# Kernel tuning notes

Measured on AMD Instinct MI355X. Metric: run time of the kernel, lower is better.

## Reference

```python
import jax, jax.numpy as jnp
import numpy as np

EPS = 1e-5
N_DOMAINS = 16


def setup_inputs() -> dict:
    key = jax.random.key(0)
    k1, k2 = jax.random.split(key)
    N, C = 65536, 512
    X = jax.random.normal(k1, (N, C), dtype=jnp.float32)
    d = jax.random.randint(k2, (N,), 0, N_DOMAINS, dtype=jnp.int32)
    parameter_t = jnp.ones((1,), dtype=jnp.float32)
    fm_mean = jnp.zeros((1, C), dtype=jnp.float32)
    gamma = jnp.ones((N_DOMAINS, C), dtype=jnp.float32)
    beta = jnp.zeros((N_DOMAINS, C), dtype=jnp.float32)
    return {"X": X, "d": d, "parameter_t": parameter_t, "fm_mean": fm_mean,
            "gamma": gamma, "beta": beta}


def reference(X, d, parameter_t, fm_mean, gamma, beta):
    # Per-domain batch normalization with dispatch/combine expressed as
    # segment reductions + gather (mathematically identical to the torch
    # loop over unique domains with mask/concat/scatter-back).
    n_domains = gamma.shape[0]
    ones = jnp.ones((X.shape[0],), dtype=X.dtype)
    cnt = jax.ops.segment_sum(ones, d, num_segments=n_domains)          # [D]
    cnt = jnp.maximum(cnt, 1.0)[:, None]                                 # [D,1]
    s = jax.ops.segment_sum(X, d, num_segments=n_domains)               # [D,C]
    sq = jax.ops.segment_sum(X * X, d, num_segments=n_domains)          # [D,C]
    mean = s / cnt                                                       # [D,C]
    var = sq / cnt - mean * mean                                         # biased var, [D,C]
    inv = jax.lax.rsqrt(var + EPS)                                       # [D,C]
    # gather per-sample domain stats and normalize (scatter-back is implicit)
    y = (X - mean[d]) * inv[d] * gamma[d] + beta[d]
    return y
```

## Files before the change

### kernel.cpp

```cpp
#include <hip/hip_runtime.h>

constexpr int   ND_  = 16;
constexpr int   C_   = 512;
constexpr float EPS_ = 1e-5f;

__global__ __launch_bounds__(256) void k_stats(
    const float2* __restrict__ X2, const int* __restrict__ dd,
    float* __restrict__ part_sum, float* __restrict__ part_sq,
    int* __restrict__ pcnt, int rows_per_chunk, int N) {
  __shared__ float2 ssum[2][ND_][128];
  __shared__ float2 ssq [2][ND_][128];
  __shared__ int    sd[256];
  __shared__ int    scnt[ND_];

  const int tid  = threadIdx.x;
  const int g    = tid >> 7;
  const int lane = tid & 127;
  const int bx   = blockIdx.x;
  const int by   = blockIdx.y;

  for (int i = tid; i < 2 * ND_ * 128; i += 256) {
    ((float2*)ssum)[i] = make_float2(0.f, 0.f);
    ((float2*)ssq )[i] = make_float2(0.f, 0.f);
  }
  if (tid < ND_) scnt[tid] = 0;
  __syncthreads();

  const int r0 = by * rows_per_chunk;
  const int r1 = min(N, r0 + rows_per_chunk);
  const int nr = r1 - r0;

  for (int i = tid; i < nr; i += 256) {
    const int v = dd[r0 + i];
    sd[i] = v;
    if (bx == 0) atomicAdd(&scnt[v], 1);
  }
  __syncthreads();

  const int jr0 = g * 128;
  const int jr1 = min(nr, jr0 + 128);
  const int ch2 = bx * 128 + lane;
  #pragma unroll 8
  for (int j = jr0; j < jr1; ++j) {
    const int    dn = sd[j];
    const float2 v  = X2[(size_t)(r0 + j) * (C_ / 2) + ch2];
    float2 a = ssum[g][dn][lane];
    a.x += v.x; a.y += v.y;
    ssum[g][dn][lane] = a;
    float2 b = ssq[g][dn][lane];
    b.x = fmaf(v.x, v.x, b.x);
    b.y = fmaf(v.y, v.y, b.y);
    ssq[g][dn][lane] = b;
  }
  __syncthreads();

  if (tid < 128) {
    #pragma unroll
    for (int dom = 0; dom < ND_; ++dom) {
      float2 a = ssum[0][dom][tid], a1 = ssum[1][dom][tid];
      a.x += a1.x; a.y += a1.y;
      ssum[0][dom][tid] = a;
      float2 b = ssq[0][dom][tid], b1 = ssq[1][dom][tid];
      b.x += b1.x; b.y += b1.y;
      ssq[0][dom][tid] = b;
    }
  }
  __syncthreads();

  float2* ps = (float2*)part_sum;
  float2* pq = (float2*)part_sq;
  const size_t base = (size_t)by * ND_ * (C_ / 2);
  for (int idx = tid; idx < ND_ * 128; idx += 256) {
    const int dom = idx >> 7;
    const int ln  = idx & 127;
    const size_t o = base + dom * (C_ / 2) + bx * 128 + ln;
    ps[o] = ssum[0][dom][ln];
    pq[o] = ssq [0][dom][ln];
  }
  if (bx == 0 && tid < ND_) pcnt[by * ND_ + tid] = scnt[tid];
}

__global__ __launch_bounds__(256) void k_finalize(
    const float* __restrict__ part_sum, const float* __restrict__ part_sq,
    const int* __restrict__ pcnt, const float* __restrict__ gamma,
    const float* __restrict__ beta, float* __restrict__ scale,
    float* __restrict__ shift, int nchunk) {
  __shared__ float ssum[8][32];
  __shared__ float ssq [8][32];
  __shared__ int   scnt[8];

  const int t     = threadIdx.x;
  const int lane  = t & 31;
  const int seg   = t >> 5;
  const int out0  = blockIdx.x * 32;
  const int gid   = out0 + lane;
  const int dom   = out0 >> 9;
  const int c     = gid & (C_ - 1);
  const int cpl   = (nchunk + 7) / 8;

  float s = 0.f, q = 0.f;
  int   cn = 0;
  for (int k = 0; k < cpl; ++k) {
    const int ch = seg * cpl + k;
    if (ch < nchunk) {
      const size_t o = ((size_t)ch * ND_ + dom) * C_ + c;
      s += part_sum[o];
      q += part_sq[o];
      cn += pcnt[ch * ND_ + dom];
    }
  }
  ssum[seg][lane] = s;
  ssq [seg][lane] = q;
  if (lane == 0) scnt[seg] = cn;
  __syncthreads();

  if (t < 32) {
    float S = 0.f, Q = 0.f;
    #pragma unroll
    for (int sg = 0; sg < 8; ++sg) { S += ssum[sg][t]; Q += ssq[sg][t]; }
    int CN = 0;
    #pragma unroll
    for (int sg = 0; sg < 8; ++sg) CN += scnt[sg];
    const float fc   = fmaxf((float)CN, 1.f);
    const float mean = S / fc;
    const float var  = Q / fc - mean * mean;
    const float inv  = rsqrtf(var + EPS_);
    const int   g    = out0 + t;
    const float sc   = inv * gamma[g];
    scale[g] = sc;
    shift[g] = fmaf(-mean, sc, beta[g]);
  }
}

__global__ __launch_bounds__(256) void k_norm(
    const float4* __restrict__ X4, const int* __restrict__ dd,
    const float4* __restrict__ scale4, const float4* __restrict__ shift4,
    float4* __restrict__ Y4, int total4) {
  int i = blockIdx.x * 256 + threadIdx.x;
  const int stride = gridDim.x * 256;
  for (; i < total4; i += stride) {
    const int n  = i >> 7;
    const int c4 = i & 127;
    const int dn = dd[n];
    const float4 x  = X4[i];
    const float4 sc = scale4[dn * (C_ / 4) + c4];
    const float4 sh = shift4[dn * (C_ / 4) + c4];
    float4 y;
    y.x = fmaf(x.x, sc.x, sh.x);
    y.y = fmaf(x.y, sc.y, sh.y);
    y.z = fmaf(x.z, sc.z, sh.z);
    y.w = fmaf(x.w, sc.w, sh.w);
    Y4[i] = y;
  }
}

extern "C" void kernel_launch(void* const* d_in, const int* in_sizes, int n_in,
                              void* d_out, int out_size, void* d_ws, size_t ws_size,
                              hipStream_t stream) {
  const float* X     = (const float*)d_in[0];
  const int*   dd    = (const int*)  d_in[1];
  const float* gamma = (const float*)d_in[4];
  const float* beta  = (const float*)d_in[5];
  float*       out   = (float*)d_out;

  const int N      = in_sizes[1];
  const int rpc    = 256;
  const int NCHUNK = (N + rpc - 1) / rpc;

  float* part_sum = out;
  float* part_sq  = out + (size_t)NCHUNK * ND_ * C_;
  int*   pcnt     = (int*)(part_sq + (size_t)NCHUNK * ND_ * C_);
  float* scale = (float*)d_ws;
  float* shift = scale + ND_ * C_;

  dim3 g1(2, NCHUNK);
  k_stats<<<g1, 256, 0, stream>>>((const float2*)X, dd, part_sum, part_sq,
                                  pcnt, rpc, N);
  k_finalize<<<(ND_ * C_) / 32, 256, 0, stream>>>(
      part_sum, part_sq, pcnt, gamma, beta, scale, shift, NCHUNK);

  const int total4 = N * (C_ / 4);
  int blocks = (total4 + 255) / 256;
  if (blocks > 2048) blocks = 2048;
  k_norm<<<blocks, 256, 0, stream>>>((const float4*)X, dd,
                                     (const float4*)scale,
                                     (const float4*)shift,
                                     (float4*)out, total4);
}
```

Measured before the change: 84.52 us.

## Replace per-chunk partial buffers with replicated atomic accumulators

Statistics blocks now atomically add their per-domain sums and squared sums into 8 replicated accumulator copies instead of writing full per-chunk partials. The finalize kernel only reduces 8 copies and reads a global count. This removes tens of megabytes of partial-sum writes and reads between kernels. In exchange it adds a memset, contention on atomics, and nondeterministic float summation order.

```diff
diff --git a/kernel.cpp b/kernel.cpp
--- a/kernel.cpp
+++ b/kernel.cpp
@@ -3,11 +3,12 @@
 constexpr int   ND_  = 16;
 constexpr int   C_   = 512;
 constexpr float EPS_ = 1e-5f;
+constexpr int   NREP = 8;
 
 __global__ __launch_bounds__(256) void k_stats(
     const float2* __restrict__ X2, const int* __restrict__ dd,
-    float* __restrict__ part_sum, float* __restrict__ part_sq,
-    int* __restrict__ pcnt, int rows_per_chunk, int N) {
+    float* __restrict__ acc_sum, float* __restrict__ acc_sq,
+    int* __restrict__ cnt, int rows_per_chunk, int N) {
   __shared__ float2 ssum[2][ND_][128];
   __shared__ float2 ssq [2][ND_][128];
   __shared__ int    sd[256];
@@ -67,69 +68,39 @@
   }
   __syncthreads();
 
-  float2* ps = (float2*)part_sum;
-  float2* pq = (float2*)part_sq;
-  const size_t base = (size_t)by * ND_ * (C_ / 2);
-  for (int idx = tid; idx < ND_ * 128; idx += 256) {
-    const int dom = idx >> 7;
-    const int ln  = idx & 127;
-    const size_t o = base + dom * (C_ / 2) + bx * 128 + ln;
-    ps[o] = ssum[0][dom][ln];
-    pq[o] = ssq [0][dom][ln];
+  float* asum = acc_sum + (size_t)(by & (NREP - 1)) * ND_ * C_;
+  float* asq  = acc_sq  + (size_t)(by & (NREP - 1)) * ND_ * C_;
+  for (int idx = tid; idx < ND_ * 256; idx += 256) {
+    const int dom = idx >> 8;
+    const int ci  = idx & 255;
+    const float sv = ((const float*)ssum[0][dom])[ci];
+    const float qv = ((const float*)ssq [0][dom])[ci];
+    unsafeAtomicAdd(&asum[dom * C_ + bx * 256 + ci], sv);
+    unsafeAtomicAdd(&asq [dom * C_ + bx * 256 + ci], qv);
   }
-  if (bx == 0 && tid < ND_) pcnt[by * ND_ + tid] = scnt[tid];
+  if (bx == 0 && tid < ND_) atomicAdd(&cnt[tid], scnt[tid]);
 }
 
-__global__ __launch_bounds__(256) void k_finalize(
-    const float* __restrict__ part_sum, const float* __restrict__ part_sq,
-    const int* __restrict__ pcnt, const float* __restrict__ gamma,
+__global__ __launch_bounds__(128) void k_finalize(
+    const float* __restrict__ acc_sum, const float* __restrict__ acc_sq,
+    const int* __restrict__ cnt, const float* __restrict__ gamma,
     const float* __restrict__ beta, float* __restrict__ scale,
-    float* __restrict__ shift, int nchunk) {
-  __shared__ float ssum[8][32];
-  __shared__ float ssq [8][32];
-  __shared__ int   scnt[8];
-
-  const int t     = threadIdx.x;
-  const int lane  = t & 31;
-  const int seg   = t >> 5;
-  const int out0  = blockIdx.x * 32;
-  const int gid   = out0 + lane;
-  const int dom   = out0 >> 9;
-  const int c     = gid & (C_ - 1);
-  const int cpl   = (nchunk + 7) / 8;
-
+    float* __restrict__ shift) {
+  const int gid = blockIdx.x * 128 + threadIdx.x;
+  const int dom = gid >> 9;
   float s = 0.f, q = 0.f;
-  int   cn = 0;
-  for (int k = 0; k < cpl; ++k) {
-    const int ch = seg * cpl + k;
-    if (ch < nchunk) {
-      const size_t o = ((size_t)ch * ND_ + dom) * C_ + c;
-      s += part_sum[o];
-      q += part_sq[o];
-      cn += pcnt[ch * ND_ + dom];
-    }
+  #pragma unroll
+  for (int r = 0; r < NREP; ++r) {
+    s += acc_sum[(size_t)r * ND_ * C_ + gid];
+    q += acc_sq [(size_t)r * ND_ * C_ + gid];
   }
-  ssum[seg][lane] = s;
-  ssq [seg][lane] = q;
-  if (lane == 0) scnt[seg] = cn;
-  __syncthreads();
-
-  if (t < 32) {
-    float S = 0.f, Q = 0.f;
-    #pragma unroll
-    for (int sg = 0; sg < 8; ++sg) { S += ssum[sg][t]; Q += ssq[sg][t]; }
-    int CN = 0;
-    #pragma unroll
-    for (int sg = 0; sg < 8; ++sg) CN += scnt[sg];
-    const float fc   = fmaxf((float)CN, 1.f);
-    const float mean = S / fc;
-    const float var  = Q / fc - mean * mean;
-    const float inv  = rsqrtf(var + EPS_);
-    const int   g    = out0 + t;
-    const float sc   = inv * gamma[g];
-    scale[g] = sc;
-    shift[g] = fmaf(-mean, sc, beta[g]);
-  }
+  const float fc   = fmaxf((float)cnt[dom], 1.f);
+  const float mean = s / fc;
+  const float var  = q / fc - mean * mean;
+  const float inv  = rsqrtf(var + EPS_);
+  const float sc   = inv * gamma[gid];
+  scale[gid] = sc;
+  shift[gid] = fmaf(-mean, sc, beta[gid]);
 }
 
 __global__ __launch_bounds__(256) void k_norm(
@@ -167,17 +138,20 @@
   const int rpc    = 256;
   const int NCHUNK = (N + rpc - 1) / rpc;
 
-  float* part_sum = out;
-  float* part_sq  = out + (size_t)NCHUNK * ND_ * C_;
-  int*   pcnt     = (int*)(part_sq + (size_t)NCHUNK * ND_ * C_);
+  const size_t accN = (size_t)NREP * ND_ * C_;
+  float* acc_sum = out + (size_t)out_size - (2 * accN + 16);
+  float* acc_sq  = acc_sum + accN;
+  int*   cnt     = (int*)(acc_sq + accN);
+  hipMemsetAsync(acc_sum, 0, (2 * accN + 16) * sizeof(float), stream);
+
   float* scale = (float*)d_ws;
   float* shift = scale + ND_ * C_;
 
   dim3 g1(2, NCHUNK);
-  k_stats<<<g1, 256, 0, stream>>>((const float2*)X, dd, part_sum, part_sq,
-                                  pcnt, rpc, N);
-  k_finalize<<<(ND_ * C_) / 32, 256, 0, stream>>>(
-      part_sum, part_sq, pcnt, gamma, beta, scale, shift, NCHUNK);
+  k_stats<<<g1, 256, 0, stream>>>((const float2*)X, dd, acc_sum, acc_sq,
+                                  cnt, rpc, N);
+  k_finalize<<<(ND_ * C_) / 128, 128, 0, stream>>>(
+      acc_sum, acc_sq, cnt, gamma, beta, scale, shift);
 
   const int total4 = N * (C_ / 4);
   int blocks = (total4 + 255) / 256;
```

Result: slower. 88.26 us (+4.4%).

## Fuse stats, finalize and normalize into one cooperative kernel with grid syncs

Applied to the files above, without the earlier changes.

Replaces the three launches (stats, finalize, normalize) with a single cooperative kernel of 256 blocks × 512 threads. Grid-wide syncs separate the partial-stat, finalize and normalize phases. Each block now handles 512 rows with 4 row-groups, which halves the number of partial chunks. The aim is to remove launch gaps and the smaller per-stage tail effects. The cost is two grid barriers and a grid that is fixed to 256 blocks, which may underfill the GPU in the bandwidth-bound normalize phase.

```diff
diff --git a/kernel.cpp b/kernel.cpp
--- a/kernel.cpp
+++ b/kernel.cpp
@@ -1,36 +1,49 @@
 #include <hip/hip_runtime.h>
+#include <hip/hip_cooperative_groups.h>
+
+namespace cg = cooperative_groups;
 
 constexpr int   ND_  = 16;
 constexpr int   C_   = 512;
 constexpr float EPS_ = 1e-5f;
-
-__global__ __launch_bounds__(256) void k_stats(
+constexpr int   RPC  = 512;
+constexpr int   NBLK = 256;
+constexpr int   NTHR = 512;
+
+__global__ __launch_bounds__(NTHR, 1) void k_fused(
     const float2* __restrict__ X2, const int* __restrict__ dd,
+    const float* __restrict__ gamma, const float* __restrict__ beta,
     float* __restrict__ part_sum, float* __restrict__ part_sq,
-    int* __restrict__ pcnt, int rows_per_chunk, int N) {
-  __shared__ float2 ssum[2][ND_][128];
-  __shared__ float2 ssq [2][ND_][128];
-  __shared__ int    sd[256];
+    int* __restrict__ pcnt, float* __restrict__ scale,
+    float* __restrict__ shift, float4* __restrict__ Y4, int N) {
+  __shared__ float2 ssum[4][ND_][128];
+  __shared__ float2 ssq [4][ND_][128];
+  __shared__ int    sd[RPC];
   __shared__ int    scnt[ND_];
+  __shared__ float  fsum[16][32];
+  __shared__ float  fsq [16][32];
+  __shared__ int    fcnt[16];
 
   const int tid  = threadIdx.x;
   const int g    = tid >> 7;
   const int lane = tid & 127;
-  const int bx   = blockIdx.x;
-  const int by   = blockIdx.y;
-
-  for (int i = tid; i < 2 * ND_ * 128; i += 256) {
+  const int bid  = blockIdx.x;
+  const int bx   = bid & 1;
+  const int by   = bid >> 1;
+  const int nchunk = (N + RPC - 1) / RPC;
+
+  for (int i = tid; i < 4 * ND_ * 128; i += NTHR) {
     ((float2*)ssum)[i] = make_float2(0.f, 0.f);
     ((float2*)ssq )[i] = make_float2(0.f, 0.f);
   }
   if (tid < ND_) scnt[tid] = 0;
   __syncthreads();
 
-  const int r0 = by * rows_per_chunk;
-  const int r1 = min(N, r0 + rows_per_chunk);
+  const int r0 = by * RPC;
+  const int r1 = min(N, r0 + RPC);
   const int nr = r1 - r0;
 
-  for (int i = tid; i < nr; i += 256) {
+  for (int i = tid; i < nr; i += NTHR) {
     const int v = dd[r0 + i];
     sd[i] = v;
     if (bx == 0) atomicAdd(&scnt[v], 1);
@@ -57,133 +70,131 @@
   if (tid < 128) {
     #pragma unroll
     for (int dom = 0; dom < ND_; ++dom) {
-      float2 a = ssum[0][dom][tid], a1 = ssum[1][dom][tid];
-      a.x += a1.x; a.y += a1.y;
+      float2 a = ssum[0][dom][tid];
+      float2 b = ssq [0][dom][tid];
+      #pragma unroll
+      for (int gg = 1; gg < 4; ++gg) {
+        const float2 a1 = ssum[gg][dom][tid];
+        const float2 b1 = ssq [gg][dom][tid];
+        a.x += a1.x; a.y += a1.y;
+        b.x += b1.x; b.y += b1.y;
+      }
       ssum[0][dom][tid] = a;
-      float2 b = ssq[0][dom][tid], b1 = ssq[1][dom][tid];
-      b.x += b1.x; b.y += b1.y;
-      ssq[0][dom][tid] = b;
-    }
-  }
-  __syncthreads();
-
-  float2* ps = (float2*)part_sum;
-  float2* pq = (float2*)part_sq;
-  const size_t base = (size_t)by * ND_ * (C_ / 2);
-  for (int idx = tid; idx < ND_ * 128; idx += 256) {
-    const int dom = idx >> 7;
-    const int ln  = idx & 127;
-    const size_t o = base + dom * (C_ / 2) + bx * 128 + ln;
-    ps[o] = ssum[0][dom][ln];
-    pq[o] = ssq [0][dom][ln];
-  }
-  if (bx == 0 && tid < ND_) pcnt[by * ND_ + tid] = scnt[tid];
-}
-
-__global__ __launch_bounds__(256) void k_finalize(
-    const float* __restrict__ part_sum, const float* __restrict__ part_sq,
-    const int* __restrict__ pcnt, const float* __restrict__ gamma,
-    const float* __restrict__ beta, float* __restrict__ scale,
-    float* __restrict__ shift, int nchunk) {
-  __shared__ float ssum[8][32];
-  __shared__ float ssq [8][32];
-  __shared__ int   scnt[8];
-
-  const int t     = threadIdx.x;
-  const int lane  = t & 31;
-  const int seg   = t >> 5;
-  const int out0  = blockIdx.x * 32;
-  const int gid   = out0 + lane;
-  const int dom   = out0 >> 9;
-  const int c     = gid & (C_ - 1);
-  const int cpl   = (nchunk + 7) / 8;
-
-  float s = 0.f, q = 0.f;
-  int   cn = 0;
-  for (int k = 0; k < cpl; ++k) {
-    const int ch = seg * cpl + k;
-    if (ch < nchunk) {
-      const size_t o = ((size_t)ch * ND_ + dom) * C_ + c;
-      s += part_sum[o];
-      q += part_sq[o];
-      cn += pcnt[ch * ND_ + dom];
-    }
-  }
-  ssum[seg][lane] = s;
-  ssq [seg][lane] = q;
-  if (lane == 0) scnt[seg] = cn;
-  __syncthreads();
-
-  if (t < 32) {
-    float S = 0.f, Q = 0.f;
-    #pragma unroll
-    for (int sg = 0; sg < 8; ++sg) { S += ssum[sg][t]; Q += ssq[sg][t]; }
-    int CN = 0;
-    #pragma unroll
-    for (int sg = 0; sg < 8; ++sg) CN += scnt[sg];
-    const float fc   = fmaxf((float)CN, 1.f);
-    const float mean = S / fc;
-    const float var  = Q / fc - mean * mean;
-    const float inv  = rsqrtf(var + EPS_);
-    const int   g    = out0 + t;
-    const float sc   = inv * gamma[g];
-    scale[g] = sc;
-    shift[g] = fmaf(-mean, sc, beta[g]);
-  }
-}
-
-__global__ __launch_bounds__(256) void k_norm(
-    const float4* __restrict__ X4, const int* __restrict__ dd,
-    const float4* __restrict__ scale4, const float4* __restrict__ shift4,
-    float4* __restrict__ Y4, int total4) {
-  int i = blockIdx.x * 256 + threadIdx.x;
-  const int stride = gridDim.x * 256;
-  for (; i < total4; i += stride) {
-    const int n  = i >> 7;
-    const int c4 = i & 127;
-    const int dn = dd[n];
-    const float4 x  = X4[i];
-    const float4 sc = scale4[dn * (C_ / 4) + c4];
-    const float4 sh = shift4[dn * (C_ / 4) + c4];
-    float4 y;
-    y.x = fmaf(x.x, sc.x, sh.x);
-    y.y = fmaf(x.y, sc.y, sh.y);
-    y.z = fmaf(x.z, sc.z, sh.z);
-    y.w = fmaf(x.w, sc.w, sh.w);
-    Y4[i] = y;
+      ssq [0][dom][tid] = b;
+    }
+  }
+  __syncthreads();
+
+  {
+    float2* ps = (float2*)part_sum;
+    float2* pq = (float2*)part_sq;
+    const size_t base = (size_t)by * ND_ * (C_ / 2);
+    for (int idx = tid; idx < ND_ * 128; idx += NTHR) {
+      const int dom = idx >> 7;
+      const int ln  = idx & 127;
+      const size_t o = base + dom * (C_ / 2) + bx * 128 + ln;
+      ps[o] = ssum[0][dom][ln];
+      pq[o] = ssq [0][dom][ln];
+    }
+    if (bx == 0 && tid < ND_) pcnt[by * ND_ + tid] = scnt[tid];
+  }
+
+  __threadfence();
+  cg::this_grid().sync();
+
+  {
+    const int lane2 = tid & 31;
+    const int seg   = tid >> 5;
+    const int out0  = bid * 32;
+    const int gid   = out0 + lane2;
+    const int dom   = out0 >> 9;
+    const int c     = gid & (C_ - 1);
+    const int cpl   = (nchunk + 15) / 16;
+
+    float s = 0.f, q = 0.f;
+    int   cn = 0;
+    for (int k = 0; k < cpl; ++k) {
+      const int ch = seg * cpl + k;
+      if (ch < nchunk) {
+        const size_t o = ((size_t)ch * ND_ + dom) * C_ + c;
+        s += part_sum[o];
+        q += part_sq[o];
+        cn += pcnt[ch * ND_ + dom];
+      }
+    }
+    fsum[seg][lane2] = s;
+    fsq [seg][lane2] = q;
+    if (lane2 == 0) fcnt[seg] = cn;
+    __syncthreads();
+
+    if (tid < 32) {
+      float S = 0.f, Q = 0.f;
+      int CN = 0;
+      #pragma unroll
+      for (int sg = 0; sg < 16; ++sg) {
+        S += fsum[sg][tid];
+        Q += fsq [sg][tid];
+        CN += fcnt[sg];
+      }
+      const float fc   = fmaxf((float)CN, 1.f);
+      const float mean = S / fc;
+      const float var  = Q / fc - mean * mean;
+      const float inv  = rsqrtf(var + EPS_);
+      const int   gg   = out0 + tid;
+      const float sc   = inv * gamma[gg];
+      scale[gg] = sc;
+      shift[gg] = fmaf(-mean, sc, beta[gg]);
+    }
+  }
+
+  __threadfence();
+  cg::this_grid().sync();
+
+  {
+    const float4* X4     = (const float4*)X2;
+    const float4* scale4 = (const float4*)scale;
+    const float4* shift4 = (const float4*)shift;
+    const int total4 = N * (C_ / 4);
+    const int stride = NBLK * NTHR;
+    for (int i = bid * NTHR + tid; i < total4; i += stride) {
+      const int n  = i >> 7;
+      const int c4 = i & 127;
+      const int dn = dd[n];
+      const float4 x  = X4[i];
+      const float4 sc = scale4[dn * (C_ / 4) + c4];
+      const float4 sh = shift4[dn * (C_ / 4) + c4];
+      float4 y;
+      y.x = fmaf(x.x, sc.x, sh.x);
+      y.y = fmaf(x.y, sc.y, sh.y);
+      y.z = fmaf(x.z, sc.z, sh.z);
+      y.w = fmaf(x.w, sc.w, sh.w);
+      Y4[i] = y;
+    }
   }
 }
 
 extern "C" void kernel_launch(void* const* d_in, const int* in_sizes, int n_in,
                               void* d_out, int out_size, void* d_ws, size_t ws_size,
                               hipStream_t stream) {
-  const float* X     = (const float*)d_in[0];
-  const int*   dd    = (const int*)  d_in[1];
-  const float* gamma = (const float*)d_in[4];
-  const float* beta  = (const float*)d_in[5];
-  float*       out   = (float*)d_out;
-
-  const int N      = in_sizes[1];
-  const int rpc    = 256;
-  const int NCHUNK = (N + rpc - 1) / rpc;
+  const float2* X2    = (const float2*)d_in[0];
+  const int*    dd    = (const int*)  d_in[1];
+  const float*  gamma = (const float*)d_in[4];
+  const float*  beta  = (const float*)d_in[5];
+  float*        out   = (float*)d_out;
+
+  int N = in_sizes[1];
+  const int NCHUNK = (N + RPC - 1) / RPC;
 
   float* part_sum = out;
   float* part_sq  = out + (size_t)NCHUNK * ND_ * C_;
   int*   pcnt     = (int*)(part_sq + (size_t)NCHUNK * ND_ * C_);
   float* scale = (float*)d_ws;
   float* shift = scale + ND_ * C_;
-
-  dim3 g1(2, NCHUNK);
-  k_stats<<<g1, 256, 0, stream>>>((const float2*)X, dd, part_sum, part_sq,
-                                  pcnt, rpc, N);
-  k_finalize<<<(ND_ * C_) / 32, 256, 0, stream>>>(
-      part_sum, part_sq, pcnt, gamma, beta, scale, shift, NCHUNK);
-
-  const int total4 = N * (C_ / 4);
-  int blocks = (total4 + 255) / 256;
-  if (blocks > 2048) blocks = 2048;
-  k_norm<<<blocks, 256, 0, stream>>>((const float4*)X, dd,
-                                     (const float4*)scale,
-                                     (const float4*)shift,
-                                     (float4*)out, total4);
+  float4* Y4 = (float4*)out;
+
+  void* args[] = {(void*)&X2, (void*)&dd, (void*)&gamma, (void*)&beta,
+                  (void*)&part_sum, (void*)&part_sq, (void*)&pcnt,
+                  (void*)&scale, (void*)&shift, (void*)&Y4, (void*)&N};
+  hipLaunchCooperativeKernel((const void*)k_fused, dim3(NBLK), dim3(NTHR),
+                             args, 0, stream);
 }
```

Measured after the change: 206.3 us. 2.44x slower.

## Retile stats kernel: 512-row chunks, 64-lane channel slices, four row groups

Applied to the files above, without the earlier changes.

The stats kernel now handles 512 rows per chunk and 64 float2 channels per block, with four 128-row groups per block, and launches four blocks per chunk in x. Each chunk now writes half as many partial sums, and the finalize kernel reduces half as many chunks. Each block keeps about the same shared-memory footprint and does the same per-thread work. Per-row-group partials now merge four ways instead of two, and the domain index array is read by four blocks per chunk instead of two.

```diff
diff --git a/kernel.cpp b/kernel.cpp
--- a/kernel.cpp
+++ b/kernel.cpp
@@ -3,31 +3,32 @@
 constexpr int   ND_  = 16;
 constexpr int   C_   = 512;
 constexpr float EPS_ = 1e-5f;
+constexpr int   RPC  = 512;
 
 __global__ __launch_bounds__(256) void k_stats(
     const float2* __restrict__ X2, const int* __restrict__ dd,
     float* __restrict__ part_sum, float* __restrict__ part_sq,
-    int* __restrict__ pcnt, int rows_per_chunk, int N) {
-  __shared__ float2 ssum[2][ND_][128];
-  __shared__ float2 ssq [2][ND_][128];
-  __shared__ int    sd[256];
+    int* __restrict__ pcnt, int N) {
+  __shared__ float2 ssum[4][ND_][64];
+  __shared__ float2 ssq [4][ND_][64];
+  __shared__ int    sd[RPC];
   __shared__ int    scnt[ND_];
 
   const int tid  = threadIdx.x;
-  const int g    = tid >> 7;
-  const int lane = tid & 127;
+  const int g    = tid >> 6;
+  const int lane = tid & 63;
   const int bx   = blockIdx.x;
   const int by   = blockIdx.y;
 
-  for (int i = tid; i < 2 * ND_ * 128; i += 256) {
+  for (int i = tid; i < 4 * ND_ * 64; i += 256) {
     ((float2*)ssum)[i] = make_float2(0.f, 0.f);
     ((float2*)ssq )[i] = make_float2(0.f, 0.f);
   }
   if (tid < ND_) scnt[tid] = 0;
   __syncthreads();
 
-  const int r0 = by * rows_per_chunk;
-  const int r1 = min(N, r0 + rows_per_chunk);
+  const int r0 = by * RPC;
+  const int r1 = min(N, r0 + RPC);
   const int nr = r1 - r0;
 
   for (int i = tid; i < nr; i += 256) {
@@ -39,7 +40,7 @@
 
   const int jr0 = g * 128;
   const int jr1 = min(nr, jr0 + 128);
-  const int ch2 = bx * 128 + lane;
+  const int ch2 = bx * 64 + lane;
   #pragma unroll 8
   for (int j = jr0; j < jr1; ++j) {
     const int    dn = sd[j];
@@ -54,26 +55,30 @@
   }
   __syncthreads();
 
-  if (tid < 128) {
+  for (int idx = tid; idx < ND_ * 64; idx += 256) {
+    const int dom = idx >> 6;
+    const int ln  = idx & 63;
+    float2 a = ssum[0][dom][ln];
+    float2 b = ssq [0][dom][ln];
     #pragma unroll
-    for (int dom = 0; dom < ND_; ++dom) {
-      float2 a = ssum[0][dom][tid], a1 = ssum[1][dom][tid];
+    for (int gg = 1; gg < 4; ++gg) {
+      const float2 a1 = ssum[gg][dom][ln];
+      const float2 b1 = ssq [gg][dom][ln];
       a.x += a1.x; a.y += a1.y;
-      ssum[0][dom][tid] = a;
-      float2 b = ssq[0][dom][tid], b1 = ssq[1][dom][tid];
       b.x += b1.x; b.y += b1.y;
-      ssq[0][dom][tid] = b;
     }
+    ssum[0][dom][ln] = a;
+    ssq [0][dom][ln] = b;
   }
   __syncthreads();
 
   float2* ps = (float2*)part_sum;
   float2* pq = (float2*)part_sq;
   const size_t base = (size_t)by * ND_ * (C_ / 2);
-  for (int idx = tid; idx < ND_ * 128; idx += 256) {
-    const int dom = idx >> 7;
-    const int ln  = idx & 127;
-    const size_t o = base + dom * (C_ / 2) + bx * 128 + ln;
+  for (int idx = tid; idx < ND_ * 64; idx += 256) {
+    const int dom = idx >> 6;
+    const int ln  = idx & 63;
+    const size_t o = base + dom * (C_ / 2) + bx * 64 + ln;
     ps[o] = ssum[0][dom][ln];
     pq[o] = ssq [0][dom][ln];
   }
@@ -164,8 +169,7 @@
   float*       out   = (float*)d_out;
 
   const int N      = in_sizes[1];
-  const int rpc    = 256;
-  const int NCHUNK = (N + rpc - 1) / rpc;
+  const int NCHUNK = (N + RPC - 1) / RPC;
 
   float* part_sum = out;
   float* part_sq  = out + (size_t)NCHUNK * ND_ * C_;
@@ -173,9 +177,9 @@
   float* scale = (float*)d_ws;
   float* shift = scale + ND_ * C_;
 
-  dim3 g1(2, NCHUNK);
+  dim3 g1(4, NCHUNK);
   k_stats<<<g1, 256, 0, stream>>>((const float2*)X, dd, part_sum, part_sq,
-                                  pcnt, rpc, N);
+                                  pcnt, N);
   k_finalize<<<(ND_ * C_) / 32, 256, 0, stream>>>(
       part_sum, part_sq, pcnt, gamma, beta, scale, shift, NCHUNK);
 
```

Result: faster. 78.28 us (-7.4%).
